# Optimization experiments

Hardware: AMD Instinct MI355X
Metric: run time of the kernel (lower is better)

The kernel has to match this reference:

```python
import jax, jax.numpy as jnp
import numpy as np

# ---- config (matches init_kwargs) ----
DIM = 1024
HEADS = 8            # local_heads == heads
QK_HD = 128          # qk_head_dim
V_HD = 128           # v_head_dim
NOPE = 64            # qk_nope_head_dim
ROPE = 64            # qk_rope_head_dim
KV_LORA = 256
N_EXP = 32
N_GROUPS = 8
TOPK = 4             # n_activated_experts
TOPK_GROUPS = 4
INTER = 512
N_SHARED = 1
ROUTE_SCALE = 1.0
EPS = 1e-6


def rmsnorm(x, w):
    xf = x.astype(jnp.float32)
    rms = jnp.sqrt(jnp.mean(xf ** 2, axis=-1, keepdims=True) + EPS)
    return (xf / rms * w).astype(x.dtype)


def setup_inputs() -> dict:
    key = jax.random.key(0)
    ks = jax.random.split(key, 16)
    s = 0.02
    return {
        "x": jax.random.normal(ks[0], (2, 1024, DIM), jnp.float32),
        # attention sub-layer params
        "norm_attn": jnp.ones((DIM,), jnp.float32),
        "wq": jax.random.normal(ks[1], (DIM, HEADS * QK_HD), jnp.float32) * s,
        "wkv_a": jax.random.normal(ks[2], (DIM, KV_LORA + ROPE), jnp.float32) * s,
        "kv_norm_w": jnp.ones((KV_LORA,), jnp.float32),
        "wkv_b": jax.random.normal(ks[3], (KV_LORA, HEADS * (NOPE + V_HD)), jnp.float32) * s,
        "wo": jax.random.normal(ks[4], (HEADS * V_HD, DIM), jnp.float32) * s,
        # MoE sub-layer params
        "norm_moe": jnp.ones((DIM,), jnp.float32),
        "gate_w": jax.random.normal(ks[5], (N_EXP, DIM), jnp.float32) * 0.01,
        "gate_b": jnp.zeros((N_EXP,), jnp.float32),
        "ew1": jax.random.normal(ks[6], (N_EXP, DIM, INTER), jnp.float32) * s,
        "ew2": jax.random.normal(ks[7], (N_EXP, INTER, DIM), jnp.float32) * s,
        "ew3": jax.random.normal(ks[8], (N_EXP, DIM, INTER), jnp.float32) * s,
        "sw1": jax.random.normal(ks[9], (DIM, N_SHARED * INTER), jnp.float32) * s,
        "sw2": jax.random.normal(ks[10], (N_SHARED * INTER, DIM), jnp.float32) * s,
        "sw3": jax.random.normal(ks[11], (DIM, N_SHARED * INTER), jnp.float32) * s,
    }


def _mla(x, wq, wkv_a, kv_norm_w, wkv_b, wo):
    B, S, _ = x.shape
    # q_lora_rank == 0 -> direct q projection; nope/rope split+concat is identity
    q = (x @ wq).reshape(B, S, HEADS, QK_HD)
    kv = x @ wkv_a                                   # [B,S,KV_LORA+ROPE]
    c, k_pe = kv[..., :KV_LORA], kv[..., KV_LORA:]
    kvp = (rmsnorm(c, kv_norm_w) @ wkv_b).reshape(B, S, HEADS, NOPE + V_HD)
    k_nope, v = kvp[..., :NOPE], kvp[..., NOPE:]
    k = jnp.concatenate(
        [k_nope, jnp.broadcast_to(k_pe[:, :, None, :], (B, S, HEADS, ROPE))], axis=-1)
    out = jax.nn.dot_product_attention(q, k, v, scale=QK_HD ** -0.5, is_causal=True)
    return out.reshape(B, S, -1) @ wo


def _gate(xf, gate_w, gate_b):
    T = xf.shape[0]
    scores = jax.nn.sigmoid(xf @ gate_w.T)           # [T,E]
    original = scores
    s = scores + gate_b
    # hierarchical group selection: top-2 score sum per group, keep top groups
    sg = s.reshape(T, N_GROUPS, -1)
    group_score = jnp.sort(sg, axis=-1)[..., -2:].sum(axis=-1)
    group_idx = jnp.argsort(group_score, axis=-1)[..., -TOPK_GROUPS:]
    mask = jnp.ones((T, N_GROUPS), bool).at[jnp.arange(T)[:, None], group_idx].set(False)
    s = jnp.where(mask[..., None], -jnp.inf, sg).reshape(T, -1)
    indices = jnp.argsort(s, axis=-1)[..., -TOPK:]   # [T,K]
    w = jnp.take_along_axis(original, indices, axis=1)
    w = w / (w.sum(axis=-1, keepdims=True) + 1e-20)  # sigmoid normalization
    return w * ROUTE_SCALE, indices


def _moe(xf, gate_w, gate_b, ew1, ew2, ew3, sw1, sw2, sw3):
    # dense all-expert SwiGLU as in the original (nn.vmap over axis_size=E)
    weights, indices = _gate(xf, gate_w, gate_b)
    h = jax.nn.silu(jnp.einsum('td,edh->eth', xf, ew1)) * jnp.einsum('td,edh->eth', xf, ew3)
    all_out = jnp.einsum('eth,ehd->etd', h, ew2)     # [E,T,dim]
    # per-token gather of its top-k experts, weighted combine
    selected = jnp.take_along_axis(all_out.transpose(1, 0, 2), indices[:, :, None], axis=1)  # [T,K,dim]
    y = (selected * weights[..., None]).sum(axis=1)
    z = (jax.nn.silu(xf @ sw1) * (xf @ sw3)) @ sw2   # shared expert MLP
    return y + z


def reference(x, norm_attn, wq, wkv_a, kv_norm_w, wkv_b, wo,
              norm_moe, gate_w, gate_b, ew1, ew2, ew3, sw1, sw2, sw3):
    # MLA layer: x + MLA(RMSNorm(x))
    x = x + _mla(rmsnorm(x, norm_attn), wq, wkv_a, kv_norm_w, wkv_b, wo)
    # MoE layer: x + MoE(RMSNorm(x))
    shape = x.shape
    xf = rmsnorm(x, norm_moe).reshape(-1, DIM)
    y = _moe(xf, gate_w, gate_b, ew1, ew2, ew3, sw1, sw2, sw3)
    return x + y.reshape(shape)
```

## Files before the change

kernel.cpp:

```cpp
#include <hip/hip_runtime.h>
#include <hip/hip_bf16.h>

#define T_TOK 2048
#define DIM 1024
#define HEADS 8
#define QK_HD 128
#define V_HD 128
#define NOPE 64
#define ROPE 64
#define KV_LORA 256
#define N_EXP 32
#define TOPK 4
#define INTER 512
#define S_LEN 1024
#define KVP_W (HEADS * (NOPE + V_HD))

typedef __attribute__((ext_vector_type(8))) _Float16 f16x8;
typedef __attribute__((ext_vector_type(4))) float f32x4;

__device__ inline unsigned short f2h(float f) {
  union { _Float16 h; unsigned short u; } c;
  c.h = (_Float16)f;
  return c.u;
}
__device__ inline float h2f(unsigned short u) {
  union { _Float16 h; unsigned short u; } c;
  c.u = u;
  return (float)c.h;
}

__launch_bounds__(256)
__global__ void tcvt_k(const float* __restrict__ src, unsigned short* __restrict__ dst,
                       int K, int N) {
  int e = blockIdx.z;
  src += (size_t)e * K * N;
  dst += (size_t)e * K * N;
  int n0 = blockIdx.x * 32, k0 = blockIdx.y * 32;
  __shared__ float ts[32][33];
  int tid = threadIdx.x;
  int r = tid >> 3, c4 = (tid & 7) * 4;
  float4 v = *(const float4*)(src + (size_t)(k0 + r) * N + n0 + c4);
  ts[r][c4] = v.x; ts[r][c4 + 1] = v.y; ts[r][c4 + 2] = v.z; ts[r][c4 + 3] = v.w;
  __syncthreads();
  ushort4 o;
  o.x = f2h(ts[c4][r]);
  o.y = f2h(ts[c4 + 1][r]);
  o.z = f2h(ts[c4 + 2][r]);
  o.w = f2h(ts[c4 + 3][r]);
  *(ushort4*)(dst + (size_t)(n0 + r) * K + k0 + c4) = o;
}

__launch_bounds__(64)
__global__ void zero_counters_k(int* __restrict__ counts, int* __restrict__ fill) {
  int i = threadIdx.x;
  if (i < N_EXP) { counts[i] = 0; fill[i] = 0; }
}

__launch_bounds__(256)
__global__ void rmsnorm_k(const float* __restrict__ x, int in_stride, int width,
                          const float* __restrict__ w, unsigned short* __restrict__ out,
                          float* __restrict__ out2, int out_stride) {
  int row = blockIdx.x;
  const float* xr = x + (size_t)row * in_stride;
  float ss = 0.f;
  for (int i = threadIdx.x; i < width; i += 256) { float v = xr[i]; ss += v * v; }
  #pragma unroll
  for (int off = 32; off; off >>= 1) ss += __shfl_down(ss, off, 64);
  __shared__ float red[4];
  if ((threadIdx.x & 63) == 0) red[threadIdx.x >> 6] = ss;
  __syncthreads();
  if (threadIdx.x == 0) {
    float tot = red[0] + red[1] + red[2] + red[3];
    red[0] = rsqrtf(tot / (float)width + 1e-6f);
  }
  __syncthreads();
  float scale = red[0];
  for (int i = threadIdx.x; i < width; i += 256) {
    float v = xr[i] * scale * w[i];
    out[(size_t)row * out_stride + i] = f2h(v);
    if (out2) out2[(size_t)row * out_stride + i] = v;
  }
}

template <int RES, int OUTH>
__launch_bounds__(256)
__global__ void gemm_bt_k(const unsigned short* __restrict__ A,
                          const unsigned short* __restrict__ B,
                          const float* __restrict__ R, void* __restrict__ Cout,
                          int N, int K) {
  const int n0 = blockIdx.x * 64;
  const int m0 = blockIdx.y * 64;
  __shared__ __align__(16) unsigned short As[64][72];
  __shared__ __align__(16) unsigned short Bs[64][72];
  const int tid = threadIdx.x;
  const int lane = tid & 63, wave = tid >> 6;
  const int quad = lane >> 4, lm = lane & 15;
  const int wm = (wave >> 1) * 32, wn = (wave & 1) * 32;
  f32x4 acc[2][2] = {};
  const int sr = tid >> 2, sc = tid & 3;
  const unsigned short* Ap = A + (size_t)(m0 + sr) * K;
  const unsigned short* Bp = B + (size_t)(n0 + sr) * K;
  for (int k0 = 0; k0 < K; k0 += 64) {
    f16x8 a0 = *(const f16x8*)(Ap + k0 + sc * 8);
    f16x8 a1 = *(const f16x8*)(Ap + k0 + sc * 8 + 32);
    f16x8 b0 = *(const f16x8*)(Bp + k0 + sc * 8);
    f16x8 b1 = *(const f16x8*)(Bp + k0 + sc * 8 + 32);
    __syncthreads();
    *(f16x8*)&As[sr][sc * 8] = a0;
    *(f16x8*)&As[sr][sc * 8 + 32] = a1;
    *(f16x8*)&Bs[sr][sc * 8] = b0;
    *(f16x8*)&Bs[sr][sc * 8 + 32] = b1;
    __syncthreads();
    #pragma unroll
    for (int ks = 0; ks < 2; ks++) {
      f16x8 af0 = *(const f16x8*)&As[wm + lm][ks * 32 + quad * 8];
      f16x8 af1 = *(const f16x8*)&As[wm + 16 + lm][ks * 32 + quad * 8];
      f16x8 bf0 = *(const f16x8*)&Bs[wn + lm][ks * 32 + quad * 8];
      f16x8 bf1 = *(const f16x8*)&Bs[wn + 16 + lm][ks * 32 + quad * 8];
      acc[0][0] = __builtin_amdgcn_mfma_f32_16x16x32_f16(af0, bf0, acc[0][0], 0, 0, 0);
      acc[0][1] = __builtin_amdgcn_mfma_f32_16x16x32_f16(af0, bf1, acc[0][1], 0, 0, 0);
      acc[1][0] = __builtin_amdgcn_mfma_f32_16x16x32_f16(af1, bf0, acc[1][0], 0, 0, 0);
      acc[1][1] = __builtin_amdgcn_mfma_f32_16x16x32_f16(af1, bf1, acc[1][1], 0, 0, 0);
    }
  }
  #pragma unroll
  for (int i = 0; i < 2; i++)
    #pragma unroll
    for (int j = 0; j < 2; j++) {
      int row = m0 + wm + i * 16 + quad * 4;
      int col = n0 + wn + j * 16 + lm;
      #pragma unroll
      for (int r = 0; r < 4; r++) {
        float v = acc[i][j][r];
        if (RES) v += R[(size_t)(row + r) * N + col];
        if (OUTH) ((unsigned short*)Cout)[(size_t)(row + r) * N + col] = f2h(v);
        else ((float*)Cout)[(size_t)(row + r) * N + col] = v;
      }
    }
}

__launch_bounds__(256)
__global__ void moe_up_k(const unsigned short* __restrict__ xfb,
                         const unsigned short* __restrict__ w1t,
                         const unsigned short* __restrict__ w3t,
                         unsigned short* __restrict__ hout,
                         const int* __restrict__ perm, const int* __restrict__ offs,
                         int Mfull) {
  const int e = blockIdx.z;
  int base = 0, count = Mfull;
  if (offs) { base = offs[e]; count = offs[e + 1] - base; }
  const int m0 = blockIdx.y * 64;
  if (m0 >= count) return;
  const int n0 = blockIdx.x * 64;
  const unsigned short* W1 = w1t + (size_t)e * (INTER * DIM);
  const unsigned short* W3 = w3t + (size_t)e * (INTER * DIM);
  __shared__ __align__(16) unsigned short As[64][72];
  __shared__ __align__(16) unsigned short B1s[64][72];
  __shared__ __align__(16) unsigned short B2s[64][72];
  __shared__ int toks[64];
  const int tid = threadIdx.x;
  if (tid < 64) {
    int g = m0 + tid;
    toks[tid] = (g < count) ? (perm ? (perm[base + g] >> 2) : g) : -1;
  }
  __syncthreads();
  const int lane = tid & 63, wave = tid >> 6;
  const int quad = lane >> 4, lm = lane & 15;
  const int wm = (wave >> 1) * 32, wn = (wave & 1) * 32;
  f32x4 acc1[2][2] = {};
  f32x4 acc2[2][2] = {};
  const int sr = tid >> 2, sc = tid & 3;
  const int tok = toks[sr];
  const unsigned short* Ap = xfb + (size_t)(tok < 0 ? 0 : tok) * DIM;
  const bool av = (tok >= 0);
  const unsigned short* B1p = W1 + (size_t)(n0 + sr) * DIM;
  const unsigned short* B2p = W3 + (size_t)(n0 + sr) * DIM;
  for (int k0 = 0; k0 < DIM; k0 += 64) {
    f16x8 a0 = {0,0,0,0,0,0,0,0}, a1 = {0,0,0,0,0,0,0,0};
    if (av) {
      a0 = *(const f16x8*)(Ap + k0 + sc * 8);
      a1 = *(const f16x8*)(Ap + k0 + sc * 8 + 32);
    }
    f16x8 b10 = *(const f16x8*)(B1p + k0 + sc * 8);
    f16x8 b11 = *(const f16x8*)(B1p + k0 + sc * 8 + 32);
    f16x8 b20 = *(const f16x8*)(B2p + k0 + sc * 8);
    f16x8 b21 = *(const f16x8*)(B2p + k0 + sc * 8 + 32);
    __syncthreads();
    *(f16x8*)&As[sr][sc * 8] = a0;
    *(f16x8*)&As[sr][sc * 8 + 32] = a1;
    *(f16x8*)&B1s[sr][sc * 8] = b10;
    *(f16x8*)&B1s[sr][sc * 8 + 32] = b11;
    *(f16x8*)&B2s[sr][sc * 8] = b20;
    *(f16x8*)&B2s[sr][sc * 8 + 32] = b21;
    __syncthreads();
    #pragma unroll
    for (int ks = 0; ks < 2; ks++) {
      f16x8 af0 = *(const f16x8*)&As[wm + lm][ks * 32 + quad * 8];
      f16x8 af1 = *(const f16x8*)&As[wm + 16 + lm][ks * 32 + quad * 8];
      f16x8 b1f0 = *(const f16x8*)&B1s[wn + lm][ks * 32 + quad * 8];
      f16x8 b1f1 = *(const f16x8*)&B1s[wn + 16 + lm][ks * 32 + quad * 8];
      f16x8 b2f0 = *(const f16x8*)&B2s[wn + lm][ks * 32 + quad * 8];
      f16x8 b2f1 = *(const f16x8*)&B2s[wn + 16 + lm][ks * 32 + quad * 8];
      acc1[0][0] = __builtin_amdgcn_mfma_f32_16x16x32_f16(af0, b1f0, acc1[0][0], 0, 0, 0);
      acc1[0][1] = __builtin_amdgcn_mfma_f32_16x16x32_f16(af0, b1f1, acc1[0][1], 0, 0, 0);
      acc1[1][0] = __builtin_amdgcn_mfma_f32_16x16x32_f16(af1, b1f0, acc1[1][0], 0, 0, 0);
      acc1[1][1] = __builtin_amdgcn_mfma_f32_16x16x32_f16(af1, b1f1, acc1[1][1], 0, 0, 0);
      acc2[0][0] = __builtin_amdgcn_mfma_f32_16x16x32_f16(af0, b2f0, acc2[0][0], 0, 0, 0);
      acc2[0][1] = __builtin_amdgcn_mfma_f32_16x16x32_f16(af0, b2f1, acc2[0][1], 0, 0, 0);
      acc2[1][0] = __builtin_amdgcn_mfma_f32_16x16x32_f16(af1, b2f0, acc2[1][0], 0, 0, 0);
      acc2[1][1] = __builtin_amdgcn_mfma_f32_16x16x32_f16(af1, b2f1, acc2[1][1], 0, 0, 0);
    }
  }
  #pragma unroll
  for (int i = 0; i < 2; i++)
    #pragma unroll
    for (int j = 0; j < 2; j++) {
      int col = n0 + wn + j * 16 + lm;
      #pragma unroll
      for (int r = 0; r < 4; r++) {
        int g = m0 + wm + i * 16 + quad * 4 + r;
        if (g < count) {
          float u = acc1[i][j][r];
          float vv = acc2[i][j][r];
          float h = (u / (1.f + __expf(-u))) * vv;
          hout[(size_t)(base + g) * INTER + col] = f2h(h);
        }
      }
    }
}

__launch_bounds__(256)
__global__ void moe_down_k(const unsigned short* __restrict__ hbuf,
                           const unsigned short* __restrict__ w2t,
                           unsigned short* __restrict__ dout,
                           const int* __restrict__ offs, int Mfull) {
  const int e = blockIdx.z;
  int base = 0, count = Mfull;
  if (offs) { base = offs[e]; count = offs[e + 1] - base; }
  const int m0 = blockIdx.y * 64;
  if (m0 >= count) return;
  const int n0 = blockIdx.x * 64;
  const unsigned short* W2 = w2t + (size_t)e * (DIM * INTER);
  __shared__ __align__(16) unsigned short As[64][72];
  __shared__ __align__(16) unsigned short Bs[64][72];
  const int tid = threadIdx.x;
  const int lane = tid & 63, wave = tid >> 6;
  const int quad = lane >> 4, lm = lane & 15;
  const int wm = (wave >> 1) * 32, wn = (wave & 1) * 32;
  f32x4 acc[2][2] = {};
  const int sr = tid >> 2, sc = tid & 3;
  const int g_s = m0 + sr;
  const bool av = (g_s < count);
  const unsigned short* Ap = hbuf + (size_t)(base + (av ? g_s : 0)) * INTER;
  const unsigned short* Bp = W2 + (size_t)(n0 + sr) * INTER;
  for (int k0 = 0; k0 < INTER; k0 += 64) {
    f16x8 a0 = {0,0,0,0,0,0,0,0}, a1 = {0,0,0,0,0,0,0,0};
    if (av) {
      a0 = *(const f16x8*)(Ap + k0 + sc * 8);
      a1 = *(const f16x8*)(Ap + k0 + sc * 8 + 32);
    }
    f16x8 b0 = *(const f16x8*)(Bp + k0 + sc * 8);
    f16x8 b1 = *(const f16x8*)(Bp + k0 + sc * 8 + 32);
    __syncthreads();
    *(f16x8*)&As[sr][sc * 8] = a0;
    *(f16x8*)&As[sr][sc * 8 + 32] = a1;
    *(f16x8*)&Bs[sr][sc * 8] = b0;
    *(f16x8*)&Bs[sr][sc * 8 + 32] = b1;
    __syncthreads();
    #pragma unroll
    for (int ks = 0; ks < 2; ks++) {
      f16x8 af0 = *(const f16x8*)&As[wm + lm][ks * 32 + quad * 8];
      f16x8 af1 = *(const f16x8*)&As[wm + 16 + lm][ks * 32 + quad * 8];
      f16x8 bf0 = *(const f16x8*)&Bs[wn + lm][ks * 32 + quad * 8];
      f16x8 bf1 = *(const f16x8*)&Bs[wn + 16 + lm][ks * 32 + quad * 8];
      acc[0][0] = __builtin_amdgcn_mfma_f32_16x16x32_f16(af0, bf0, acc[0][0], 0, 0, 0);
      acc[0][1] = __builtin_amdgcn_mfma_f32_16x16x32_f16(af0, bf1, acc[0][1], 0, 0, 0);
      acc[1][0] = __builtin_amdgcn_mfma_f32_16x16x32_f16(af1, bf0, acc[1][0], 0, 0, 0);
      acc[1][1] = __builtin_amdgcn_mfma_f32_16x16x32_f16(af1, bf1, acc[1][1], 0, 0, 0);
    }
  }
  #pragma unroll
  for (int i = 0; i < 2; i++)
    #pragma unroll
    for (int j = 0; j < 2; j++) {
      int col = n0 + wn + j * 16 + lm;
      #pragma unroll
      for (int r = 0; r < 4; r++) {
        int g = m0 + wm + i * 16 + quad * 4 + r;
        if (g < count)
          dout[(size_t)(base + g) * DIM + col] = f2h(acc[i][j][r]);
      }
    }
}

__launch_bounds__(256)
__global__ void attn_k(const unsigned short* __restrict__ q,
                       const unsigned short* __restrict__ kvp,
                       const float* __restrict__ kvb,
                       unsigned short* __restrict__ o) {
  const int qt = blockIdx.x, h = blockIdx.y, b = blockIdx.z;
  __shared__ __align__(16) _Float16 Qs[64][136];
  __shared__ __align__(16) _Float16 Ks[64][136];
  __shared__ __align__(16) _Float16 Vt[128][72];
  __shared__ __align__(16) _Float16 Ps[4][16][72];
  const int tid = threadIdx.x;
  const int lane = tid & 63, wave = tid >> 6;
  const int quad = lane >> 4, lm = lane & 15;
  const int qr0 = wave * 16;
  const float scale = 0.08838834764831845f;
  const int tq = b * S_LEN + qt * 64;

  for (int i = tid; i < 64 * 16; i += 256) {
    int row = i & 63, g = i >> 6;
    *(f16x8*)&Qs[row][g * 8] =
        *(const f16x8*)(q + (size_t)(tq + row) * 1024 + h * 128 + g * 8);
  }

  float m_i[4], l_i[4];
  #pragma unroll
  for (int r = 0; r < 4; r++) { m_i[r] = -1e30f; l_i[r] = 0.f; }
  f32x4 o_acc[8] = {};

  for (int kt = 0; kt <= qt; ++kt) {
    const int tk = b * S_LEN + kt * 64;
    for (int i = tid; i < 64 * 8; i += 256) {
      int key = i & 63, g = i >> 6;
      *(f16x8*)&Ks[key][g * 8] =
          *(const f16x8*)(kvp + (size_t)(tk + key) * KVP_W + h * 192 + g * 8);
    }
    for (int i = tid; i < 64 * 16; i += 256) {
      int key = i & 63, g = i >> 6;
      float4 v = *(const float4*)(kvb + (size_t)(tk + key) * 320 + 256 + g * 4);
      ushort4 u;
      u.x = f2h(v.x); u.y = f2h(v.y); u.z = f2h(v.z); u.w = f2h(v.w);
      *(ushort4*)&Ks[key][64 + g * 4] = u;
    }
    for (int i = tid; i < 64 * 16; i += 256) {
      int key = i & 63, g = i >> 6;
      f16x8 v = *(const f16x8*)(kvp + (size_t)(tk + key) * KVP_W + h * 192 + 64 + g * 8);
      #pragma unroll
      for (int j = 0; j < 8; j++) Vt[g * 8 + j][key] = v[j];
    }
    __syncthreads();

    f32x4 sacc[4] = {};
    #pragma unroll
    for (int kc = 0; kc < 4; kc++) {
      f16x8 af = *(const f16x8*)&Qs[qr0 + lm][kc * 32 + quad * 8];
      #pragma unroll
      for (int jn = 0; jn < 4; jn++) {
        f16x8 bf = *(const f16x8*)&Ks[jn * 16 + lm][kc * 32 + quad * 8];
        sacc[jn] = __builtin_amdgcn_mfma_f32_16x16x32_f16(af, bf, sacc[jn], 0, 0, 0);
      }
    }
    const bool diag = (kt == qt);
    float p[4][4];
    float rowmax[4], rowsum[4];
    #pragma unroll
    for (int r = 0; r < 4; r++) rowmax[r] = -1e30f;
    #pragma unroll
    for (int jn = 0; jn < 4; jn++)
      #pragma unroll
      for (int r = 0; r < 4; r++) {
        float s = sacc[jn][r] * scale;
        if (diag && (jn * 16 + lm > qr0 + quad * 4 + r)) s = -1e30f;
        p[jn][r] = s;
        rowmax[r] = fmaxf(rowmax[r], s);
      }
    #pragma unroll
    for (int m = 1; m < 16; m <<= 1)
      #pragma unroll
      for (int r = 0; r < 4; r++)
        rowmax[r] = fmaxf(rowmax[r], __shfl_xor(rowmax[r], m, 64));
    float al[4];
    #pragma unroll
    for (int r = 0; r < 4; r++) {
      float mn = fmaxf(m_i[r], rowmax[r]);
      al[r] = __expf(m_i[r] - mn);
      m_i[r] = mn;
      rowsum[r] = 0.f;
    }
    #pragma unroll
    for (int jn = 0; jn < 4; jn++)
      #pragma unroll
      for (int r = 0; r < 4; r++) {
        float pv = __expf(p[jn][r] - m_i[r]);
        p[jn][r] = pv;
        rowsum[r] += pv;
      }
    #pragma unroll
    for (int m = 1; m < 16; m <<= 1)
      #pragma unroll
      for (int r = 0; r < 4; r++)
        rowsum[r] += __shfl_xor(rowsum[r], m, 64);
    #pragma unroll
    for (int r = 0; r < 4; r++) l_i[r] = l_i[r] * al[r] + rowsum[r];
    #pragma unroll
    for (int jn2 = 0; jn2 < 8; jn2++)
      #pragma unroll
      for (int r = 0; r < 4; r++) o_acc[jn2][r] *= al[r];
    #pragma unroll
    for (int jn = 0; jn < 4; jn++)
      #pragma unroll
      for (int r = 0; r < 4; r++)
        Ps[wave][quad * 4 + r][jn * 16 + lm] = (_Float16)p[jn][r];
    #pragma unroll
    for (int kc = 0; kc < 2; kc++) {
      f16x8 af = *(const f16x8*)&Ps[wave][lm][kc * 32 + quad * 8];
      #pragma unroll
      for (int jn2 = 0; jn2 < 8; jn2++) {
        f16x8 bf = *(const f16x8*)&Vt[jn2 * 16 + lm][kc * 32 + quad * 8];
        o_acc[jn2] = __builtin_amdgcn_mfma_f32_16x16x32_f16(af, bf, o_acc[jn2], 0, 0, 0);
      }
    }
    __syncthreads();
  }
  #pragma unroll
  for (int r = 0; r < 4; r++) l_i[r] = 1.f / l_i[r];
  #pragma unroll
  for (int jn2 = 0; jn2 < 8; jn2++) {
    int col = h * 128 + jn2 * 16 + lm;
    #pragma unroll
    for (int r = 0; r < 4; r++) {
      int row = tq + qr0 + quad * 4 + r;
      o[(size_t)row * 1024 + col] = f2h(o_acc[jn2][r] * l_i[r]);
    }
  }
}

__launch_bounds__(256)
__global__ void gate_k(const float* __restrict__ xf, const float* __restrict__ gw,
                       const float* __restrict__ gb, float* __restrict__ tw,
                       int* __restrict__ tidx, int* __restrict__ counts) {
  int t = blockIdx.x;
  __shared__ float xs[DIM];
  __shared__ float part[256];
  __shared__ float sc[N_EXP];
  int tid = threadIdx.x;
  for (int i = tid; i < DIM; i += 256) xs[i] = xf[(size_t)t * DIM + i];
  __syncthreads();
  {
    int e = tid >> 3, p = tid & 7;
    float s = 0.f;
    const float* ge = gw + (size_t)e * DIM + p * 128;
    const float* xp = xs + p * 128;
    for (int d = 0; d < 128; d++) s += xp[d] * ge[d];
    part[tid] = s;
  }
  __syncthreads();
  if (tid < N_EXP) {
    float tot = 0.f;
    for (int p = 0; p < 8; p++) tot += part[tid * 8 + p];
    sc[tid] = 1.f / (1.f + __expf(-tot));
  }
  __syncthreads();
  if (tid == 0) {
    float orig[N_EXP], sb[N_EXP];
    for (int i = 0; i < N_EXP; i++) { orig[i] = sc[i]; sb[i] = orig[i] + gb[i]; }
    float gsc[8];
    for (int g = 0; g < 8; g++) {
      float m1 = -1e30f, m2 = -1e30f;
      for (int j = 0; j < 4; j++) {
        float v = sb[g * 4 + j];
        if (v > m1) { m2 = m1; m1 = v; } else if (v > m2) m2 = v;
      }
      gsc[g] = m1 + m2;
    }
    bool gok[8] = {false, false, false, false, false, false, false, false};
    for (int it = 0; it < 4; it++) {
      int best = 0; float bv = -1e30f;
      for (int g = 0; g < 8; g++)
        if (!gok[g] && gsc[g] >= bv) { bv = gsc[g]; best = g; }
      gok[best] = true;
    }
    bool taken[N_EXP] = {};
    int idx[TOPK]; float wsum = 0.f;
    for (int k = 0; k < TOPK; k++) {
      int best = 0; float bv = -1e30f;
      for (int i = 0; i < N_EXP; i++)
        if (gok[i >> 2] && !taken[i] && sb[i] >= bv) { bv = sb[i]; best = i; }
      taken[best] = true; idx[k] = best; wsum += orig[best];
    }
    float inv = 1.f / (wsum + 1e-20f);
    for (int k = 0; k < TOPK; k++) {
      tidx[t * TOPK + k] = idx[k];
      tw[t * TOPK + k] = orig[idx[k]] * inv;
      atomicAdd(&counts[idx[k]], 1);
    }
  }
}

__global__ void scan_k(const int* __restrict__ counts, int* __restrict__ offs) {
  if (threadIdx.x == 0 && blockIdx.x == 0) {
    int acc = 0;
    for (int e = 0; e < N_EXP; e++) { offs[e] = acc; acc += counts[e]; }
    offs[N_EXP] = acc;
  }
}

__launch_bounds__(256)
__global__ void scatter_k(const int* __restrict__ tidx, const int* __restrict__ offs,
                          int* __restrict__ fill, int* __restrict__ perm,
                          int* __restrict__ posOf) {
  int t = blockIdx.x * 256 + threadIdx.x;
  if (t >= T_TOK) return;
  for (int j = 0; j < TOPK; j++) {
    int e = tidx[t * TOPK + j];
    int pos = atomicAdd(&fill[e], 1);
    int p = offs[e] + pos;
    perm[p] = t * TOPK + j;
    posOf[t * TOPK + j] = p;
  }
}

__launch_bounds__(256)
__global__ void final_gather_k(const float* __restrict__ x1,
                               const unsigned short* __restrict__ dbuf,
                               const unsigned short* __restrict__ sdbuf,
                               const int* __restrict__ posOf,
                               const float* __restrict__ tw,
                               float* __restrict__ out) {
  int t = blockIdx.x;
  int c0 = threadIdx.x * 4;
  int p0 = posOf[t * 4 + 0], p1 = posOf[t * 4 + 1];
  int p2 = posOf[t * 4 + 2], p3 = posOf[t * 4 + 3];
  float w0 = tw[t * 4 + 0], w1 = tw[t * 4 + 1];
  float w2 = tw[t * 4 + 2], w3 = tw[t * 4 + 3];
  size_t tb = (size_t)t * DIM;
  #pragma unroll
  for (int i = 0; i < 4; i++) {
    int c = c0 + i;
    float v = x1[tb + c] + h2f(sdbuf[tb + c])
            + w0 * h2f(dbuf[(size_t)p0 * DIM + c])
            + w1 * h2f(dbuf[(size_t)p1 * DIM + c])
            + w2 * h2f(dbuf[(size_t)p2 * DIM + c])
            + w3 * h2f(dbuf[(size_t)p3 * DIM + c]);
    out[tb + c] = v;
  }
}

extern "C" void kernel_launch(void* const* d_in, const int* in_sizes, int n_in,
                              void* d_out, int out_size, void* d_ws, size_t ws_size,
                              hipStream_t stream) {
  const float* x        = (const float*)d_in[0];
  const float* norm_attn= (const float*)d_in[1];
  const float* wq       = (const float*)d_in[2];
  const float* wkv_a    = (const float*)d_in[3];
  const float* kv_norm_w= (const float*)d_in[4];
  const float* wkv_b    = (const float*)d_in[5];
  const float* wo       = (const float*)d_in[6];
  const float* norm_moe = (const float*)d_in[7];
  const float* gate_w   = (const float*)d_in[8];
  const float* gate_b   = (const float*)d_in[9];
  const float* ew1      = (const float*)d_in[10];
  const float* ew2      = (const float*)d_in[11];
  const float* ew3      = (const float*)d_in[12];
  const float* sw1      = (const float*)d_in[13];
  const float* sw2      = (const float*)d_in[14];
  const float* sw3      = (const float*)d_in[15];
  float* out = (float*)d_out;

  char* wp = (char*)d_ws;
  auto alloc = [&](size_t bytes) -> char* {
    char* r = wp;
    wp += (bytes + 255) & ~(size_t)255;
    return r;
  };
  typedef unsigned short us;
  us* wqT   = (us*)alloc(1048576 * 2);
  us* wkvaT = (us*)alloc(327680 * 2);
  us* wkvbT = (us*)alloc(393216 * 2);
  us* woT   = (us*)alloc(1048576 * 2);
  us* ew1T  = (us*)alloc((size_t)16777216 * 2);
  us* ew3T  = (us*)alloc((size_t)16777216 * 2);
  us* ew2T  = (us*)alloc((size_t)16777216 * 2);
  us* sw1T  = (us*)alloc(524288 * 2);
  us* sw3T  = (us*)alloc(524288 * 2);
  us* sw2T  = (us*)alloc(524288 * 2);
  us* xb    = (us*)alloc(2097152 * 2);
  us* cn    = (us*)alloc(524288 * 2);
  us* atn   = (us*)alloc(2097152 * 2);
  us* dbuf  = (us*)alloc((size_t)8388608 * 2);
  us* qb    = (us*)alloc(2097152 * 4);
  float* kvb  = (float*)alloc(655360 * 4);
  us* kvp   = (us*)alloc(3145728 * 4);
  float* x1   = (float*)alloc(2097152 * 4);
  float* xf32 = (float*)alloc(2097152 * 4);
  float* twb  = (float*)alloc(8192 * 4);
  int* tidx   = (int*)alloc(8192 * 4);
  int* perm   = (int*)alloc(8192 * 4);
  int* posOf  = (int*)alloc(8192 * 4);
  int* counts = (int*)alloc(64 * 4);
  int* offs   = (int*)alloc(64 * 4);
  int* fill   = (int*)alloc(64 * 4);
  us* sdbuf = qb;
  us* hbuf  = kvp;
  us* hs    = hbuf + (size_t)8192 * 512;

  tcvt_k<<<dim3(32, 32, 1), 256, 0, stream>>>(wq, wqT, 1024, 1024);
  tcvt_k<<<dim3(10, 32, 1), 256, 0, stream>>>(wkv_a, wkvaT, 1024, 320);
  tcvt_k<<<dim3(48, 8, 1), 256, 0, stream>>>(wkv_b, wkvbT, 256, 1536);
  tcvt_k<<<dim3(32, 32, 1), 256, 0, stream>>>(wo, woT, 1024, 1024);
  tcvt_k<<<dim3(16, 32, 32), 256, 0, stream>>>(ew1, ew1T, 1024, 512);
  tcvt_k<<<dim3(16, 32, 32), 256, 0, stream>>>(ew3, ew3T, 1024, 512);
  tcvt_k<<<dim3(32, 16, 32), 256, 0, stream>>>(ew2, ew2T, 512, 1024);
  tcvt_k<<<dim3(16, 32, 1), 256, 0, stream>>>(sw1, sw1T, 1024, 512);
  tcvt_k<<<dim3(16, 32, 1), 256, 0, stream>>>(sw3, sw3T, 1024, 512);
  tcvt_k<<<dim3(32, 16, 1), 256, 0, stream>>>(sw2, sw2T, 512, 1024);

  rmsnorm_k<<<T_TOK, 256, 0, stream>>>(x, DIM, DIM, norm_attn, xb, nullptr, DIM);
  gemm_bt_k<0, 1><<<dim3(16, 32), 256, 0, stream>>>(xb, wqT, nullptr, qb, 1024, 1024);
  gemm_bt_k<0, 0><<<dim3(5, 32), 256, 0, stream>>>(xb, wkvaT, nullptr, kvb, 320, 1024);
  rmsnorm_k<<<T_TOK, 256, 0, stream>>>(kvb, 320, KV_LORA, kv_norm_w, cn, nullptr, KV_LORA);
  gemm_bt_k<0, 1><<<dim3(24, 32), 256, 0, stream>>>(cn, wkvbT, nullptr, kvp, 1536, 256);
  attn_k<<<dim3(S_LEN / 64, HEADS, 2), 256, 0, stream>>>(qb, kvp, kvb, atn);
  gemm_bt_k<1, 0><<<dim3(16, 32), 256, 0, stream>>>(atn, woT, x, x1, 1024, 1024);

  rmsnorm_k<<<T_TOK, 256, 0, stream>>>(x1, DIM, DIM, norm_moe, xb, xf32, DIM);
  zero_counters_k<<<1, 64, 0, stream>>>(counts, fill);
  gate_k<<<T_TOK, 256, 0, stream>>>(xf32, gate_w, gate_b, twb, tidx, counts);
  scan_k<<<1, 1, 0, stream>>>(counts, offs);
  scatter_k<<<(T_TOK + 255) / 256, 256, 0, stream>>>(tidx, offs, fill, perm, posOf);
  moe_up_k<<<dim3(8, 32, 32), 256, 0, stream>>>(xb, ew1T, ew3T, hbuf, perm, offs, 0);
  moe_down_k<<<dim3(16, 32, 32), 256, 0, stream>>>(hbuf, ew2T, dbuf, offs, 0);
  moe_up_k<<<dim3(8, 32, 1), 256, 0, stream>>>(xb, sw1T, sw3T, hs, nullptr, nullptr, T_TOK);
  moe_down_k<<<dim3(16, 32, 1), 256, 0, stream>>>(hs, sw2T, sdbuf, nullptr, T_TOK);

  final_gather_k<<<T_TOK, 256, 0, stream>>>(x1, dbuf, sdbuf, posOf, twb, out);
}
```

Measured before the change: 600.6 us.

## Split gating into tiled score GEMM and per-thread routing kernel

The per-token gate kernel, which reloaded the gate weights for every token and ran top-k selection on a single thread, is replaced by two kernels. The first is a tiled kernel that computes gate logits for 32 tokens per block from shared memory, so each weight tile is reused across tokens. The second runs sigmoid, group selection and top-k with one thread per token using bitmasks in registers. This adds an intermediate score buffer and an extra launch in exchange for better weight reuse and more parallel routing.

```diff
diff --git a/kernel.cpp b/kernel.cpp
--- a/kernel.cpp
+++ b/kernel.cpp
@@ -429,64 +429,92 @@
 }
 
 __launch_bounds__(256)
-__global__ void gate_k(const float* __restrict__ xf, const float* __restrict__ gw,
-                       const float* __restrict__ gb, float* __restrict__ tw,
-                       int* __restrict__ tidx, int* __restrict__ counts) {
-  int t = blockIdx.x;
-  __shared__ float xs[DIM];
-  __shared__ float part[256];
-  __shared__ float sc[N_EXP];
-  int tid = threadIdx.x;
-  for (int i = tid; i < DIM; i += 256) xs[i] = xf[(size_t)t * DIM + i];
-  __syncthreads();
-  {
-    int e = tid >> 3, p = tid & 7;
-    float s = 0.f;
-    const float* ge = gw + (size_t)e * DIM + p * 128;
-    const float* xp = xs + p * 128;
-    for (int d = 0; d < 128; d++) s += xp[d] * ge[d];
-    part[tid] = s;
-  }
-  __syncthreads();
-  if (tid < N_EXP) {
-    float tot = 0.f;
-    for (int p = 0; p < 8; p++) tot += part[tid * 8 + p];
-    sc[tid] = 1.f / (1.f + __expf(-tot));
-  }
-  __syncthreads();
-  if (tid == 0) {
-    float orig[N_EXP], sb[N_EXP];
-    for (int i = 0; i < N_EXP; i++) { orig[i] = sc[i]; sb[i] = orig[i] + gb[i]; }
-    float gsc[8];
-    for (int g = 0; g < 8; g++) {
-      float m1 = -1e30f, m2 = -1e30f;
-      for (int j = 0; j < 4; j++) {
-        float v = sb[g * 4 + j];
-        if (v > m1) { m2 = m1; m1 = v; } else if (v > m2) m2 = v;
-      }
-      gsc[g] = m1 + m2;
-    }
-    bool gok[8] = {false, false, false, false, false, false, false, false};
+__global__ void scores_k(const float* __restrict__ xf, const float* __restrict__ gw,
+                         float* __restrict__ sc) {
+  __shared__ float xls[32][129];
+  __shared__ float gls[32][129];
+  const int t0 = blockIdx.x * 32;
+  const int tid = threadIdx.x;
+  const int lr = tid >> 3, lc = tid & 7;
+  const int e = tid & 31, tg = tid >> 5;
+  float acc[4] = {};
+  for (int k0 = 0; k0 < DIM; k0 += 128) {
+    __syncthreads();
+    #pragma unroll
     for (int it = 0; it < 4; it++) {
-      int best = 0; float bv = -1e30f;
-      for (int g = 0; g < 8; g++)
-        if (!gok[g] && gsc[g] >= bv) { bv = gsc[g]; best = g; }
-      gok[best] = true;
-    }
-    bool taken[N_EXP] = {};
-    int idx[TOPK]; float wsum = 0.f;
-    for (int k = 0; k < TOPK; k++) {
-      int best = 0; float bv = -1e30f;
-      for (int i = 0; i < N_EXP; i++)
-        if (gok[i >> 2] && !taken[i] && sb[i] >= bv) { bv = sb[i]; best = i; }
-      taken[best] = true; idx[k] = best; wsum += orig[best];
-    }
-    float inv = 1.f / (wsum + 1e-20f);
-    for (int k = 0; k < TOPK; k++) {
-      tidx[t * TOPK + k] = idx[k];
-      tw[t * TOPK + k] = orig[idx[k]] * inv;
-      atomicAdd(&counts[idx[k]], 1);
-    }
+      int col = lc * 4 + it * 32;
+      *(float4*)&xls[lr][col] = *(const float4*)(xf + (size_t)(t0 + lr) * DIM + k0 + col);
+      *(float4*)&gls[lr][col] = *(const float4*)(gw + (size_t)lr * DIM + k0 + col);
+    }
+    __syncthreads();
+    for (int d = 0; d < 128; d++) {
+      float g = gls[e][d];
+      #pragma unroll
+      for (int j = 0; j < 4; j++)
+        acc[j] += xls[tg * 4 + j][d] * g;
+    }
+  }
+  #pragma unroll
+  for (int j = 0; j < 4; j++)
+    sc[(size_t)(t0 + tg * 4 + j) * N_EXP + e] = acc[j];
+}
+
+__launch_bounds__(64)
+__global__ void route_k(const float* __restrict__ sc, const float* __restrict__ gb,
+                        float* __restrict__ tw, int* __restrict__ tidx,
+                        int* __restrict__ counts) {
+  int t = blockIdx.x * 64 + threadIdx.x;
+  if (t >= T_TOK) return;
+  float orig[N_EXP], sb[N_EXP];
+  #pragma unroll
+  for (int i = 0; i < N_EXP; i++) {
+    float s = 1.f / (1.f + __expf(-sc[(size_t)t * N_EXP + i]));
+    orig[i] = s;
+    sb[i] = s + gb[i];
+  }
+  float gsc[8];
+  #pragma unroll
+  for (int g = 0; g < 8; g++) {
+    float m1 = -1e30f, m2 = -1e30f;
+    #pragma unroll
+    for (int j = 0; j < 4; j++) {
+      float v = sb[g * 4 + j];
+      if (v > m1) { m2 = m1; m1 = v; } else if (v > m2) m2 = v;
+    }
+    gsc[g] = m1 + m2;
+  }
+  unsigned gok = 0;
+  #pragma unroll
+  for (int it = 0; it < 4; it++) {
+    int best = 0; float bv = -1e30f;
+    #pragma unroll
+    for (int g = 0; g < 8; g++)
+      if (!((gok >> g) & 1u) && gsc[g] >= bv) { bv = gsc[g]; best = g; }
+    gok |= 1u << best;
+  }
+  unsigned emask = 0;
+  #pragma unroll
+  for (int g = 0; g < 8; g++)
+    if ((gok >> g) & 1u) emask |= 0xFu << (g * 4);
+  unsigned taken = 0;
+  int idx[TOPK]; float ow[TOPK]; float wsum = 0.f;
+  #pragma unroll
+  for (int k = 0; k < TOPK; k++) {
+    int best = 0; float bv = -1e30f, bo = 0.f;
+    #pragma unroll
+    for (int i = 0; i < N_EXP; i++)
+      if (((emask >> i) & 1u) && !((taken >> i) & 1u) && sb[i] >= bv) {
+        bv = sb[i]; best = i; bo = orig[i];
+      }
+    taken |= 1u << best;
+    idx[k] = best; ow[k] = bo; wsum += bo;
+  }
+  float inv = 1.f / (wsum + 1e-20f);
+  #pragma unroll
+  for (int k = 0; k < TOPK; k++) {
+    tidx[t * TOPK + k] = idx[k];
+    tw[t * TOPK + k] = ow[k] * inv;
+    atomicAdd(&counts[idx[k]], 1);
   }
 }
 
@@ -586,6 +614,7 @@
   us* kvp   = (us*)alloc(3145728 * 4);
   float* x1   = (float*)alloc(2097152 * 4);
   float* xf32 = (float*)alloc(2097152 * 4);
+  float* scb  = (float*)alloc(65536 * 4);
   float* twb  = (float*)alloc(8192 * 4);
   int* tidx   = (int*)alloc(8192 * 4);
   int* perm   = (int*)alloc(8192 * 4);
@@ -618,7 +647,8 @@
 
   rmsnorm_k<<<T_TOK, 256, 0, stream>>>(x1, DIM, DIM, norm_moe, xb, xf32, DIM);
   zero_counters_k<<<1, 64, 0, stream>>>(counts, fill);
-  gate_k<<<T_TOK, 256, 0, stream>>>(xf32, gate_w, gate_b, twb, tidx, counts);
+  scores_k<<<T_TOK / 32, 256, 0, stream>>>(xf32, gate_w, scb);
+  route_k<<<T_TOK / 64, 64, 0, stream>>>(scb, gate_b, twb, tidx, counts);
   scan_k<<<1, 1, 0, stream>>>(counts, offs);
   scatter_k<<<(T_TOK + 255) / 256, 256, 0, stream>>>(tidx, offs, fill, perm, posOf);
   moe_up_k<<<dim3(8, 32, 32), 256, 0, stream>>>(xb, ew1T, ew3T, hbuf, perm, offs, 0);
```

Result: faster. 583.2 us (-2.9%).
